# Kernel tuning notes

Measured on AMD Instinct MI355X. Metric: run time of the kernel, lower is better.

## Reference

```python
import jax, jax.numpy as jnp
import numpy as np

N = 100000   # nodes
E = 640000   # edges
D = 128      # in_channels
C = 40       # out_channels (classes)


def setup_inputs() -> dict:
    key = jax.random.key(0)
    ks = jax.random.split(key, 6)
    x = jax.random.normal(ks[0], (N, D), jnp.float32)
    edge_index = jax.random.randint(ks[1], (2, E), 0, N)
    edge_weight = jax.random.uniform(ks[2], (E,), jnp.float32)
    # 8 block convs (4 blocks x 2) stacked, + final conv
    Wb = jax.random.normal(ks[3], (8, D, D), jnp.float32) / np.sqrt(D)
    bb = jnp.zeros((8, D), jnp.float32)
    Wf = jax.random.normal(ks[4], (D, C), jnp.float32) / np.sqrt(D)
    bf = jnp.zeros((C,), jnp.float32)
    return dict(x=x, edge_index=edge_index, edge_weight=edge_weight,
                Wb=Wb, bb=bb, Wf=Wf, bf=bf)


def _gcn(x, W, b, src, dst, w):
    """PyG GCNConv (normalize=True) with self-loops already appended to src/dst/w."""
    n = x.shape[0]
    h = x @ W                                   # [N, out]
    deg = jax.ops.segment_sum(w, dst, num_segments=n)
    dinv = jnp.where(deg > 0, jax.lax.rsqrt(deg), 0.0)
    norm = dinv[src] * w * dinv[dst]            # [E+N]
    out = jax.ops.segment_sum(h[src] * norm[:, None], dst, num_segments=n)
    return out + b


def reference(x, edge_index, edge_weight, Wb, bb, Wf, bf):
    n = x.shape[0]
    loop = jnp.arange(n)
    src = jnp.concatenate([edge_index[0], loop])
    dst = jnp.concatenate([edge_index[1], loop])
    w = jnp.concatenate([edge_weight, jnp.ones((n,), x.dtype)])
    # forward only runs blocks 1-4 (blocks 5-7 unused in the original forward)
    for i in range(4):
        identity = x
        x = jax.nn.relu(_gcn(x, Wb[2 * i], bb[2 * i], src, dst, w))
        # dropout: identity in eval mode
        x = jax.nn.relu(_gcn(x, Wb[2 * i + 1], bb[2 * i + 1], src, dst, w))
        # F.normalize: row-wise L2 with eps=1e-12
        x = x / jnp.maximum(jnp.linalg.norm(x, axis=1, keepdims=True), 1e-12)
        x = (x + identity) / 2
    x = _gcn(x, Wf, bf, src, dst, w)
    return jax.nn.log_softmax(x, axis=1)
```

## Files before the change

kernel.cpp:

```cpp
#include <hip/hip_runtime.h>
#include <math.h>

#define NN 100000
#define EE 640000
#define DD 128
#define CC 40
#define FIXS 4194304.0f

typedef __bf16 bf16x8 __attribute__((ext_vector_type(8)));
typedef float f32x4 __attribute__((ext_vector_type(4)));
typedef unsigned short us8 __attribute__((ext_vector_type(8)));

__device__ inline unsigned short f2b(float f) {
    union { float f; unsigned u; } v; v.f = f;
    unsigned u = v.u;
    return (unsigned short)((u + 0x7FFFu + ((u >> 16) & 1u)) >> 16);
}
__device__ inline float b2f(unsigned short b) {
    union { unsigned u; float f; } v; v.u = ((unsigned)b) << 16;
    return v.f;
}


__global__ __launch_bounds__(256) void k_edge1(const int* __restrict__ dst,
                                               const float* __restrict__ w,
                                               unsigned long long* __restrict__ degcnt,
                                               int* __restrict__ pos) {
    int e = blockIdx.x * 256 + threadIdx.x;
    if (e < EE) {
        int d = dst[e];
        unsigned long long pk =
            ((unsigned long long)(unsigned)(w[e] * FIXS) << 32) | 1ull;
        unsigned long long old = atomicAdd(&degcnt[d], pk);
        pos[e] = (int)(old & 0xffffffffull);
    }
}

__global__ __launch_bounds__(256) void k_scan1(const unsigned long long* __restrict__ degcnt,
                                               float* __restrict__ dinv,
                                               int* __restrict__ out,
                                               int* __restrict__ partial) {
    __shared__ int lds[256];
    int t = threadIdx.x;
    int base = blockIdx.x * 1024 + t * 4;
    int v[4]; int s = 0;
    #pragma unroll
    for (int j = 0; j < 4; ++j) {
        int idx = base + j;
        unsigned long long dc = (idx < NN) ? degcnt[idx] : 0ull;
        v[j] = (int)(dc & 0xffffffffull);
        s += v[j];
        if (idx < NN)
            dinv[idx] = rsqrtf((float)(unsigned)(dc >> 32) * (1.0f / FIXS) + 1.0f);
    }
    lds[t] = s;
    __syncthreads();
    for (int off = 1; off < 256; off <<= 1) {
        int x = lds[t];
        int y = (t >= off) ? lds[t - off] : 0;
        __syncthreads();
        lds[t] = x + y;
        __syncthreads();
    }
    int excl = lds[t] - s;
    if (t == 255) partial[blockIdx.x] = lds[255];
    int run = excl;
    #pragma unroll
    for (int j = 0; j < 4; ++j) {
        int idx = base + j;
        if (idx < NN) out[idx] = run;
        run += v[j];
    }
}

__global__ __launch_bounds__(128) void k_scan2(int* __restrict__ partial) {
    __shared__ int lds[128];
    int t = threadIdx.x;
    int v = (t < 98) ? partial[t] : 0;
    lds[t] = v;
    __syncthreads();
    for (int off = 1; off < 128; off <<= 1) {
        int x = lds[t];
        int y = (t >= off) ? lds[t - off] : 0;
        __syncthreads();
        lds[t] = x + y;
        __syncthreads();
    }
    if (t < 98) partial[t] = lds[t] - v;
}

__global__ __launch_bounds__(256) void k_scan3(int* __restrict__ rp,
                                               const int* __restrict__ partial) {
    int i = blockIdx.x * 256 + threadIdx.x;
    if (i < NN) rp[i] += partial[i >> 10];
    if (i == 0) rp[NN] = EE;
}

__global__ __launch_bounds__(256) void k_scatter(const int* __restrict__ src,
                                                 const int* __restrict__ dst,
                                                 const float* __restrict__ w,
                                                 const float* __restrict__ dinv,
                                                 const int* __restrict__ rp,
                                                 const int* __restrict__ pos,
                                                 int* __restrict__ col,
                                                 float* __restrict__ val) {
    int e = blockIdx.x * 256 + threadIdx.x;
    if (e < EE) {
        int s = src[e], d = dst[e];
        int p = rp[d] + pos[e];
        col[p] = s;
        val[p] = dinv[s] * w[e] * dinv[d];
    }
}


__global__ __launch_bounds__(256) void k_prep_w(const float* __restrict__ Wb,
                                                unsigned short* __restrict__ WT) {
    int idx = blockIdx.x * 256 + threadIdx.x;
    if (idx >= 8 * DD * DD) return;
    int m = idx >> 14;
    int n = (idx >> 7) & 127;
    int k = idx & 127;
    WT[idx] = f2b(Wb[(size_t)m * DD * DD + (size_t)k * DD + n]);
}

__global__ __launch_bounds__(256) void k_prep_wf(const float* __restrict__ Wf,
                                                 unsigned short* __restrict__ WfT) {
    int idx = blockIdx.x * 256 + threadIdx.x;
    if (idx >= 64 * DD) return;
    int n = idx >> 7;
    int k = idx & 127;
    WfT[idx] = (n < CC) ? f2b(Wf[(size_t)k * CC + n]) : 0;
}

__global__ __launch_bounds__(256) void k_x2bf(const float* __restrict__ x,
                                              unsigned short* __restrict__ Abf) {
    int idx = blockIdx.x * 256 + threadIdx.x;
    if (idx >= NN * DD / 4) return;
    float4 v = ((const float4*)x)[idx];
    ushort4 r;
    r.x = f2b(v.x); r.y = f2b(v.y); r.z = f2b(v.z); r.w = f2b(v.w);
    ((ushort4*)Abf)[idx] = r;
}

__global__ __launch_bounds__(256) void k_mm_mfma(const unsigned short* __restrict__ X,
                                                 const unsigned short* __restrict__ WT,
                                                 unsigned short* __restrict__ H) {
    int wid = threadIdx.x >> 6;
    int lane = threadIdx.x & 63;
    int r0 = blockIdx.x * 64 + wid * 16;
    int sl = lane & 15, g = lane >> 4;
    int arow = r0 + sl;
    if (arow >= NN) arow = NN - 1;

    f32x4 acc[8];
    #pragma unroll
    for (int n = 0; n < 8; ++n) acc[n] = (f32x4){0.f, 0.f, 0.f, 0.f};

    const bf16x8* xrow = (const bf16x8*)(X + (size_t)arow * DD);
    #pragma unroll
    for (int kc = 0; kc < 4; ++kc) {
        bf16x8 a = xrow[kc * 4 + g];
        #pragma unroll
        for (int n = 0; n < 8; ++n) {
            const bf16x8* wrow = (const bf16x8*)(WT + (size_t)(n * 16 + sl) * DD);
            bf16x8 b = wrow[kc * 4 + g];
            acc[n] = __builtin_amdgcn_mfma_f32_16x16x32_bf16(a, b, acc[n], 0, 0, 0);
        }
    }
    #pragma unroll
    for (int n = 0; n < 8; ++n) {
        #pragma unroll
        for (int v = 0; v < 4; ++v) {
            int row = r0 + g * 4 + v;
            if (row < NN) H[(size_t)row * DD + n * 16 + sl] = f2b(acc[n][v]);
        }
    }
}

__global__ __launch_bounds__(256) void k_mm40b(const unsigned short* __restrict__ X,
                                               const unsigned short* __restrict__ WfT,
                                               unsigned short* __restrict__ H) {
    int wid = threadIdx.x >> 6;
    int lane = threadIdx.x & 63;
    int r0 = blockIdx.x * 64 + wid * 16;
    int sl = lane & 15, g = lane >> 4;
    int arow = r0 + sl;
    if (arow >= NN) arow = NN - 1;

    f32x4 acc[4];
    #pragma unroll
    for (int n = 0; n < 4; ++n) acc[n] = (f32x4){0.f, 0.f, 0.f, 0.f};

    const bf16x8* xrow = (const bf16x8*)(X + (size_t)arow * DD);
    #pragma unroll
    for (int kc = 0; kc < 4; ++kc) {
        bf16x8 a = xrow[kc * 4 + g];
        #pragma unroll
        for (int n = 0; n < 4; ++n) {
            const bf16x8* wrow = (const bf16x8*)(WfT + (size_t)(n * 16 + sl) * DD);
            bf16x8 b = wrow[kc * 4 + g];
            acc[n] = __builtin_amdgcn_mfma_f32_16x16x32_bf16(a, b, acc[n], 0, 0, 0);
        }
    }
    #pragma unroll
    for (int n = 0; n < 4; ++n) {
        #pragma unroll
        for (int v = 0; v < 4; ++v) {
            int row = r0 + g * 4 + v;
            if (row < NN) H[(size_t)row * 64 + n * 16 + sl] = f2b(acc[n][v]);
        }
    }
}


#define AGG_CORE(h_, node_, sl_, a_, STRIDE_)                               \
    {                                                                       \
        float dv = dinv[node_];                                             \
        float dv2 = dv * dv;                                                \
        us8 m_ = ((const us8*)(h_ + (size_t)node_ * STRIDE_))[sl_];         \
        _Pragma("unroll")                                                   \
        for (int j = 0; j < 8; ++j) a_[j] = dv2 * b2f(m_[j]);               \
        int e = rp[node_], end = rp[node_ + 1];                             \
        for (; e + 4 <= end; e += 4) {                                      \
            int s0 = col[e], s1 = col[e + 1], s2 = col[e + 2], s3 = col[e + 3]; \
            float v0 = val[e], v1 = val[e + 1], v2 = val[e + 2], v3 = val[e + 3]; \
            us8 q0 = ((const us8*)(h_ + (size_t)s0 * STRIDE_))[sl_];        \
            us8 q1 = ((const us8*)(h_ + (size_t)s1 * STRIDE_))[sl_];        \
            us8 q2 = ((const us8*)(h_ + (size_t)s2 * STRIDE_))[sl_];        \
            us8 q3 = ((const us8*)(h_ + (size_t)s3 * STRIDE_))[sl_];        \
            _Pragma("unroll")                                               \
            for (int j = 0; j < 8; ++j)                                     \
                a_[j] += (v0 * b2f(q0[j]) + v1 * b2f(q1[j]))                \
                       + (v2 * b2f(q2[j]) + v3 * b2f(q3[j]));               \
        }                                                                   \
        for (; e < end; ++e) {                                              \
            int s0 = col[e];                                                \
            float v0 = val[e];                                              \
            us8 q0 = ((const us8*)(h_ + (size_t)s0 * STRIDE_))[sl_];        \
            _Pragma("unroll")                                               \
            for (int j = 0; j < 8; ++j) a_[j] += v0 * b2f(q0[j]);           \
        }                                                                   \
    }

__global__ __launch_bounds__(256) void k_agg128(const unsigned short* __restrict__ h,
                                                const float* __restrict__ dinv,
                                                const int* __restrict__ rp,
                                                const int* __restrict__ col,
                                                const float* __restrict__ val,
                                                const float* __restrict__ bias,
                                                unsigned short* __restrict__ outb) {
    int node = blockIdx.x * 16 + (threadIdx.x >> 4);
    int sl = threadIdx.x & 15;
    if (node >= NN) return;
    float a[8];
    AGG_CORE(h, node, sl, a, DD);
    float4 bz0 = ((const float4*)bias)[sl * 2];
    float4 bz1 = ((const float4*)bias)[sl * 2 + 1];
    float bb[8] = {bz0.x, bz0.y, bz0.z, bz0.w, bz1.x, bz1.y, bz1.z, bz1.w};
    us8 r;
    #pragma unroll
    for (int j = 0; j < 8; ++j) r[j] = f2b(fmaxf(a[j] + bb[j], 0.f));
    ((us8*)(outb + (size_t)node * DD))[sl] = r;
}

__global__ __launch_bounds__(256) void k_agg128_nr(const unsigned short* __restrict__ h,
                                                   const float* __restrict__ dinv,
                                                   const int* __restrict__ rp,
                                                   const int* __restrict__ col,
                                                   const float* __restrict__ val,
                                                   const float* __restrict__ bias,
                                                   unsigned short* __restrict__ Abf) {
    int node = blockIdx.x * 16 + (threadIdx.x >> 4);
    int sl = threadIdx.x & 15;
    if (node >= NN) return;
    float a[8];
    AGG_CORE(h, node, sl, a, DD);
    float4 bz0 = ((const float4*)bias)[sl * 2];
    float4 bz1 = ((const float4*)bias)[sl * 2 + 1];
    float bb[8] = {bz0.x, bz0.y, bz0.z, bz0.w, bz1.x, bz1.y, bz1.z, bz1.w};
    float ss = 0.f;
    #pragma unroll
    for (int j = 0; j < 8; ++j) {
        a[j] = fmaxf(a[j] + bb[j], 0.f);
        ss += a[j] * a[j];
    }
    ss += __shfl_xor(ss, 1);
    ss += __shfl_xor(ss, 2);
    ss += __shfl_xor(ss, 4);
    ss += __shfl_xor(ss, 8);
    float sc = 1.0f / fmaxf(sqrtf(ss), 1e-12f);
    us8 oldb = ((const us8*)(Abf + (size_t)node * DD))[sl];
    us8 rb;
    #pragma unroll
    for (int j = 0; j < 8; ++j)
        rb[j] = f2b((a[j] * sc + b2f(oldb[j])) * 0.5f);
    ((us8*)(Abf + (size_t)node * DD))[sl] = rb;
}

__global__ __launch_bounds__(256) void k_agg_final(const unsigned short* __restrict__ h,
                                                   const float* __restrict__ dinv,
                                                   const int* __restrict__ rp,
                                                   const int* __restrict__ col,
                                                   const float* __restrict__ val,
                                                   const float* __restrict__ bias,
                                                   float* __restrict__ out) {
    int node = blockIdx.x * 32 + (threadIdx.x >> 3);
    int sl = threadIdx.x & 7;
    if (node >= NN) return;
    float a[8];
    AGG_CORE(h, node, sl, a, 64);
    bool real = sl < 5;
    float vv[8];
    if (real) {
        float4 bz0 = ((const float4*)bias)[sl * 2];
        float4 bz1 = ((const float4*)bias)[sl * 2 + 1];
        float bb[8] = {bz0.x, bz0.y, bz0.z, bz0.w, bz1.x, bz1.y, bz1.z, bz1.w};
        #pragma unroll
        for (int j = 0; j < 8; ++j) vv[j] = a[j] + bb[j];
    } else {
        #pragma unroll
        for (int j = 0; j < 8; ++j) vv[j] = -3.0e38f;
    }
    float m = vv[0];
    #pragma unroll
    for (int j = 1; j < 8; ++j) m = fmaxf(m, vv[j]);
    m = fmaxf(m, __shfl_xor(m, 1));
    m = fmaxf(m, __shfl_xor(m, 2));
    m = fmaxf(m, __shfl_xor(m, 4));
    float s = 0.f;
    if (real) {
        #pragma unroll
        for (int j = 0; j < 8; ++j) s += expf(vv[j] - m);
    }
    s += __shfl_xor(s, 1);
    s += __shfl_xor(s, 2);
    s += __shfl_xor(s, 4);
    float ls = m + logf(s);
    if (real) {
        float4 o0 = {vv[0] - ls, vv[1] - ls, vv[2] - ls, vv[3] - ls};
        float4 o1 = {vv[4] - ls, vv[5] - ls, vv[6] - ls, vv[7] - ls};
        float* orow = out + (size_t)node * CC + sl * 8;
        *(float4*)(orow) = o0;
        *(float4*)(orow + 4) = o1;
    }
}


extern "C" void kernel_launch(void* const* d_in, const int* in_sizes, int n_in,
                              void* d_out, int out_size, void* d_ws, size_t ws_size,
                              hipStream_t stream) {
    const float* x  = (const float*)d_in[0];
    const int*   ei = (const int*)d_in[1];
    const float* ew = (const float*)d_in[2];
    const float* Wb = (const float*)d_in[3];
    const float* bb = (const float*)d_in[4];
    const float* Wf = (const float*)d_in[5];
    const float* bf_ = (const float*)d_in[6];
    const int* src = ei;
    const int* dst = ei + EE;
    float* out = (float*)d_out;

    char* p = (char*)d_ws;
    unsigned short*     Abf    = (unsigned short*)p;     p += (size_t)NN * DD * 2;
    unsigned short*     Bbf    = (unsigned short*)p;     p += (size_t)NN * DD * 2;
    unsigned short*     Cbf    = (unsigned short*)p;     p += (size_t)NN * DD * 2;
    unsigned short*     H48    = (unsigned short*)p;     p += (size_t)NN * 64 * 2;
    unsigned short*     WT     = (unsigned short*)p;     p += (size_t)8 * DD * DD * 2;
    unsigned short*     WfT    = (unsigned short*)p;     p += (size_t)64 * DD * 2;
    unsigned long long* degcnt = (unsigned long long*)p; p += (size_t)NN * 8;
    float* dinv = (float*)p; p += (size_t)NN * 4;
    int*   rp   = (int*)p;   p += (size_t)(NN + 1) * 4;
    int*   pos  = (int*)p;   p += (size_t)EE * 4;
    int*   col  = (int*)p;   p += (size_t)EE * 4;
    float* val  = (float*)p; p += (size_t)EE * 4;
    int*   partial = (int*)p; p += 128 * 4;

    hipMemsetAsync(degcnt, 0, (size_t)NN * 8, stream);

    k_edge1<<<(EE + 255) / 256, 256, 0, stream>>>(dst, ew, degcnt, pos);
    k_scan1<<<98, 256, 0, stream>>>(degcnt, dinv, rp, partial);
    k_scan2<<<1, 128, 0, stream>>>(partial);
    k_scan3<<<(NN + 255) / 256, 256, 0, stream>>>(rp, partial);
    k_scatter<<<(EE + 255) / 256, 256, 0, stream>>>(src, dst, ew, dinv, rp, pos, col, val);

    k_prep_w<<<(8 * DD * DD + 255) / 256, 256, 0, stream>>>(Wb, WT);
    k_prep_wf<<<(64 * DD + 255) / 256, 256, 0, stream>>>(Wf, WfT);
    k_x2bf<<<(NN * DD / 4 + 255) / 256, 256, 0, stream>>>(x, Abf);

    for (int blk = 0; blk < 4; ++blk) {
        k_mm_mfma<<<(NN + 63) / 64, 256, 0, stream>>>(Abf, WT + (size_t)(2 * blk) * DD * DD, Bbf);
        k_agg128<<<(NN + 15) / 16, 256, 0, stream>>>(Bbf, dinv, rp, col, val, bb + (size_t)(2 * blk) * DD, Cbf);
        k_mm_mfma<<<(NN + 63) / 64, 256, 0, stream>>>(Cbf, WT + (size_t)(2 * blk + 1) * DD * DD, Bbf);
        k_agg128_nr<<<(NN + 15) / 16, 256, 0, stream>>>(Bbf, dinv, rp, col, val, bb + (size_t)(2 * blk + 1) * DD, Abf);
    }
    k_mm40b<<<(NN + 63) / 64, 256, 0, stream>>>(Abf, WfT, H48);
    k_agg_final<<<(NN + 31) / 32, 256, 0, stream>>>(H48, dinv, rp, col, val, bf_, out);
}
```

Before: 666.0 us.

## Fuse aggregation with the next layer's MFMA matmul through shared memory

Each aggregation kernel now writes its 64-node output tile into LDS and immediately multiplies it by the next layer's weight with MFMA. This removes the separate matmul kernels and the round trip of the intermediate activation through global memory. The input conversion is fused with the first matmul, and the two weight-prep kernels are merged into one. Aggregation blocks now cover 64 nodes in four serial rounds instead of 16 nodes, which lowers parallelism per block and may lengthen the tail caused by uneven node degrees.

```diff
diff --git a/kernel.cpp b/kernel.cpp
--- a/kernel.cpp
+++ b/kernel.cpp
@@ -113,105 +113,55 @@
     }
 }
 
-
-__global__ __launch_bounds__(256) void k_prep_w(const float* __restrict__ Wb,
-                                                unsigned short* __restrict__ WT) {
+__global__ __launch_bounds__(256) void k_prep(const float* __restrict__ Wb,
+                                              const float* __restrict__ Wf,
+                                              unsigned short* __restrict__ WT,
+                                              unsigned short* __restrict__ WfT) {
     int idx = blockIdx.x * 256 + threadIdx.x;
-    if (idx >= 8 * DD * DD) return;
-    int m = idx >> 14;
-    int n = (idx >> 7) & 127;
-    int k = idx & 127;
-    WT[idx] = f2b(Wb[(size_t)m * DD * DD + (size_t)k * DD + n]);
-}
-
-__global__ __launch_bounds__(256) void k_prep_wf(const float* __restrict__ Wf,
-                                                 unsigned short* __restrict__ WfT) {
-    int idx = blockIdx.x * 256 + threadIdx.x;
-    if (idx >= 64 * DD) return;
-    int n = idx >> 7;
-    int k = idx & 127;
-    WfT[idx] = (n < CC) ? f2b(Wf[(size_t)k * CC + n]) : 0;
-}
-
-__global__ __launch_bounds__(256) void k_x2bf(const float* __restrict__ x,
-                                              unsigned short* __restrict__ Abf) {
-    int idx = blockIdx.x * 256 + threadIdx.x;
-    if (idx >= NN * DD / 4) return;
-    float4 v = ((const float4*)x)[idx];
-    ushort4 r;
-    r.x = f2b(v.x); r.y = f2b(v.y); r.z = f2b(v.z); r.w = f2b(v.w);
-    ((ushort4*)Abf)[idx] = r;
-}
-
-__global__ __launch_bounds__(256) void k_mm_mfma(const unsigned short* __restrict__ X,
-                                                 const unsigned short* __restrict__ WT,
-                                                 unsigned short* __restrict__ H) {
-    int wid = threadIdx.x >> 6;
-    int lane = threadIdx.x & 63;
-    int r0 = blockIdx.x * 64 + wid * 16;
-    int sl = lane & 15, g = lane >> 4;
-    int arow = r0 + sl;
-    if (arow >= NN) arow = NN - 1;
-
-    f32x4 acc[8];
-    #pragma unroll
-    for (int n = 0; n < 8; ++n) acc[n] = (f32x4){0.f, 0.f, 0.f, 0.f};
-
-    const bf16x8* xrow = (const bf16x8*)(X + (size_t)arow * DD);
-    #pragma unroll
-    for (int kc = 0; kc < 4; ++kc) {
-        bf16x8 a = xrow[kc * 4 + g];
-        #pragma unroll
-        for (int n = 0; n < 8; ++n) {
-            const bf16x8* wrow = (const bf16x8*)(WT + (size_t)(n * 16 + sl) * DD);
-            bf16x8 b = wrow[kc * 4 + g];
-            acc[n] = __builtin_amdgcn_mfma_f32_16x16x32_bf16(a, b, acc[n], 0, 0, 0);
-        }
-    }
-    #pragma unroll
-    for (int n = 0; n < 8; ++n) {
-        #pragma unroll
-        for (int v = 0; v < 4; ++v) {
-            int row = r0 + g * 4 + v;
-            if (row < NN) H[(size_t)row * DD + n * 16 + sl] = f2b(acc[n][v]);
-        }
-    }
-}
-
-__global__ __launch_bounds__(256) void k_mm40b(const unsigned short* __restrict__ X,
-                                               const unsigned short* __restrict__ WfT,
-                                               unsigned short* __restrict__ H) {
-    int wid = threadIdx.x >> 6;
-    int lane = threadIdx.x & 63;
-    int r0 = blockIdx.x * 64 + wid * 16;
-    int sl = lane & 15, g = lane >> 4;
-    int arow = r0 + sl;
-    if (arow >= NN) arow = NN - 1;
-
-    f32x4 acc[4];
-    #pragma unroll
-    for (int n = 0; n < 4; ++n) acc[n] = (f32x4){0.f, 0.f, 0.f, 0.f};
-
-    const bf16x8* xrow = (const bf16x8*)(X + (size_t)arow * DD);
-    #pragma unroll
-    for (int kc = 0; kc < 4; ++kc) {
-        bf16x8 a = xrow[kc * 4 + g];
-        #pragma unroll
-        for (int n = 0; n < 4; ++n) {
-            const bf16x8* wrow = (const bf16x8*)(WfT + (size_t)(n * 16 + sl) * DD);
-            bf16x8 b = wrow[kc * 4 + g];
-            acc[n] = __builtin_amdgcn_mfma_f32_16x16x32_bf16(a, b, acc[n], 0, 0, 0);
-        }
-    }
-    #pragma unroll
-    for (int n = 0; n < 4; ++n) {
-        #pragma unroll
-        for (int v = 0; v < 4; ++v) {
-            int row = r0 + g * 4 + v;
-            if (row < NN) H[(size_t)row * 64 + n * 16 + sl] = f2b(acc[n][v]);
-        }
-    }
-}
+    if (idx < 8 * DD * DD) {
+        int m = idx >> 14;
+        int n = (idx >> 7) & 127;
+        int k = idx & 127;
+        WT[idx] = f2b(Wb[(size_t)m * DD * DD + (size_t)k * DD + n]);
+    } else {
+        int j = idx - 8 * DD * DD;
+        if (j < 64 * DD) {
+            int n = j >> 7;
+            int k = j & 127;
+            WfT[j] = (n < CC) ? f2b(Wf[(size_t)k * CC + n]) : 0;
+        }
+    }
+}
+
+
+#define MFMA_PHASE(WT_, H_)                                                  \
+    {                                                                        \
+        int wid = threadIdx.x >> 6;                                          \
+        int lane = threadIdx.x & 63;                                         \
+        int msl = lane & 15, g = lane >> 4;                                  \
+        int r0 = node0 + wid * 16;                                           \
+        f32x4 acc[8];                                                        \
+        _Pragma("unroll")                                                    \
+        for (int n = 0; n < 8; ++n) acc[n] = (f32x4){0.f, 0.f, 0.f, 0.f};    \
+        _Pragma("unroll")                                                    \
+        for (int kc = 0; kc < 4; ++kc) {                                     \
+            bf16x8 a = *(const bf16x8*)(&xs[wid * 16 + msl][kc * 32 + g * 8]); \
+            _Pragma("unroll")                                                \
+            for (int n = 0; n < 8; ++n) {                                    \
+                const bf16x8* wrow = (const bf16x8*)(WT_ + (size_t)(n * 16 + msl) * DD); \
+                bf16x8 b = wrow[kc * 4 + g];                                 \
+                acc[n] = __builtin_amdgcn_mfma_f32_16x16x32_bf16(a, b, acc[n], 0, 0, 0); \
+            }                                                                \
+        }                                                                    \
+        _Pragma("unroll")                                                    \
+        for (int n = 0; n < 8; ++n) {                                        \
+            _Pragma("unroll")                                                \
+            for (int v = 0; v < 4; ++v) {                                    \
+                int row = r0 + g * 4 + v;                                    \
+                if (row < NN) H_[(size_t)row * DD + n * 16 + msl] = f2b(acc[n][v]); \
+            }                                                                \
+        }                                                                    \
+    }
 
 
 #define AGG_CORE(h_, node_, sl_, a_, STRIDE_)                               \
@@ -243,25 +193,113 @@
         }                                                                   \
     }
 
-__global__ __launch_bounds__(256) void k_agg128(const unsigned short* __restrict__ h,
-                                                const float* __restrict__ dinv,
-                                                const int* __restrict__ rp,
-                                                const int* __restrict__ col,
-                                                const float* __restrict__ val,
-                                                const float* __restrict__ bias,
-                                                unsigned short* __restrict__ outb) {
-    int node = blockIdx.x * 16 + (threadIdx.x >> 4);
+
+__global__ __launch_bounds__(256) void k_xmm(const float* __restrict__ x,
+                                             const unsigned short* __restrict__ WT,
+                                             unsigned short* __restrict__ Abf,
+                                             unsigned short* __restrict__ H) {
+    __shared__ unsigned short xs[64][136];
+    int node0 = blockIdx.x * 64;
     int sl = threadIdx.x & 15;
-    if (node >= NN) return;
-    float a[8];
-    AGG_CORE(h, node, sl, a, DD);
-    float4 bz0 = ((const float4*)bias)[sl * 2];
-    float4 bz1 = ((const float4*)bias)[sl * 2 + 1];
-    float bb[8] = {bz0.x, bz0.y, bz0.z, bz0.w, bz1.x, bz1.y, bz1.z, bz1.w};
-    us8 r;
-    #pragma unroll
-    for (int j = 0; j < 8; ++j) r[j] = f2b(fmaxf(a[j] + bb[j], 0.f));
-    ((us8*)(outb + (size_t)node * DD))[sl] = r;
+    int grp = threadIdx.x >> 4;
+    for (int rnd = 0; rnd < 4; ++rnd) {
+        int node = node0 + rnd * 16 + grp;
+        us8 r;
+        if (node < NN) {
+            float4 v0 = *(const float4*)(x + (size_t)node * DD + sl * 8);
+            float4 v1 = *(const float4*)(x + (size_t)node * DD + sl * 8 + 4);
+            r[0] = f2b(v0.x); r[1] = f2b(v0.y); r[2] = f2b(v0.z); r[3] = f2b(v0.w);
+            r[4] = f2b(v1.x); r[5] = f2b(v1.y); r[6] = f2b(v1.z); r[7] = f2b(v1.w);
+            ((us8*)(Abf + (size_t)node * DD))[sl] = r;
+        } else {
+            #pragma unroll
+            for (int j = 0; j < 8; ++j) r[j] = 0;
+        }
+        *(us8*)(&xs[rnd * 16 + grp][sl * 8]) = r;
+    }
+    __syncthreads();
+    MFMA_PHASE(WT, H);
+}
+
+__global__ __launch_bounds__(256) void k_aggmm(const unsigned short* __restrict__ h,
+                                               const float* __restrict__ dinv,
+                                               const int* __restrict__ rp,
+                                               const int* __restrict__ col,
+                                               const float* __restrict__ val,
+                                               const float* __restrict__ bias,
+                                               const unsigned short* __restrict__ WTn,
+                                               unsigned short* __restrict__ H) {
+    __shared__ unsigned short xs[64][136];
+    int node0 = blockIdx.x * 64;
+    int sl = threadIdx.x & 15;
+    int grp = threadIdx.x >> 4;
+    for (int rnd = 0; rnd < 4; ++rnd) {
+        int node = node0 + rnd * 16 + grp;
+        us8 r;
+        if (node < NN) {
+            float a[8];
+            AGG_CORE(h, node, sl, a, DD);
+            float4 bz0 = ((const float4*)bias)[sl * 2];
+            float4 bz1 = ((const float4*)bias)[sl * 2 + 1];
+            float bb[8] = {bz0.x, bz0.y, bz0.z, bz0.w, bz1.x, bz1.y, bz1.z, bz1.w};
+            #pragma unroll
+            for (int j = 0; j < 8; ++j) r[j] = f2b(fmaxf(a[j] + bb[j], 0.f));
+        } else {
+            #pragma unroll
+            for (int j = 0; j < 8; ++j) r[j] = 0;
+        }
+        *(us8*)(&xs[rnd * 16 + grp][sl * 8]) = r;
+    }
+    __syncthreads();
+    MFMA_PHASE(WTn, H);
+}
+
+__global__ __launch_bounds__(256) void k_aggnr_mm(const unsigned short* __restrict__ h,
+                                                  const float* __restrict__ dinv,
+                                                  const int* __restrict__ rp,
+                                                  const int* __restrict__ col,
+                                                  const float* __restrict__ val,
+                                                  const float* __restrict__ bias,
+                                                  unsigned short* __restrict__ Abf,
+                                                  const unsigned short* __restrict__ WTn,
+                                                  unsigned short* __restrict__ H) {
+    __shared__ unsigned short xs[64][136];
+    int node0 = blockIdx.x * 64;
+    int sl = threadIdx.x & 15;
+    int grp = threadIdx.x >> 4;
+    for (int rnd = 0; rnd < 4; ++rnd) {
+        int node = node0 + rnd * 16 + grp;
+        us8 rb;
+        if (node < NN) {
+            float a[8];
+            AGG_CORE(h, node, sl, a, DD);
+            float4 bz0 = ((const float4*)bias)[sl * 2];
+            float4 bz1 = ((const float4*)bias)[sl * 2 + 1];
+            float bb[8] = {bz0.x, bz0.y, bz0.z, bz0.w, bz1.x, bz1.y, bz1.z, bz1.w};
+            float ss = 0.f;
+            #pragma unroll
+            for (int j = 0; j < 8; ++j) {
+                a[j] = fmaxf(a[j] + bb[j], 0.f);
+                ss += a[j] * a[j];
+            }
+            ss += __shfl_xor(ss, 1);
+            ss += __shfl_xor(ss, 2);
+            ss += __shfl_xor(ss, 4);
+            ss += __shfl_xor(ss, 8);
+            float sc = 1.0f / fmaxf(sqrtf(ss), 1e-12f);
+            us8 oldb = ((const us8*)(Abf + (size_t)node * DD))[sl];
+            #pragma unroll
+            for (int j = 0; j < 8; ++j)
+                rb[j] = f2b((a[j] * sc + b2f(oldb[j])) * 0.5f);
+            ((us8*)(Abf + (size_t)node * DD))[sl] = rb;
+        } else {
+            #pragma unroll
+            for (int j = 0; j < 8; ++j) rb[j] = 0;
+        }
+        *(us8*)(&xs[rnd * 16 + grp][sl * 8]) = rb;
+    }
+    __syncthreads();
+    MFMA_PHASE(WTn, H);
 }
 
 __global__ __launch_bounds__(256) void k_agg128_nr(const unsigned short* __restrict__ h,
@@ -296,6 +334,41 @@
     for (int j = 0; j < 8; ++j)
         rb[j] = f2b((a[j] * sc + b2f(oldb[j])) * 0.5f);
     ((us8*)(Abf + (size_t)node * DD))[sl] = rb;
+}
+
+__global__ __launch_bounds__(256) void k_mm40b(const unsigned short* __restrict__ X,
+                                               const unsigned short* __restrict__ WfT,
+                                               unsigned short* __restrict__ H) {
+    int wid = threadIdx.x >> 6;
+    int lane = threadIdx.x & 63;
+    int r0 = blockIdx.x * 64 + wid * 16;
+    int sl = lane & 15, g = lane >> 4;
+    int arow = r0 + sl;
+    if (arow >= NN) arow = NN - 1;
+
+    f32x4 acc[4];
+    #pragma unroll
+    for (int n = 0; n < 4; ++n) acc[n] = (f32x4){0.f, 0.f, 0.f, 0.f};
+
+    const bf16x8* xrow = (const bf16x8*)(X + (size_t)arow * DD);
+    #pragma unroll
+    for (int kc = 0; kc < 4; ++kc) {
+        bf16x8 a = xrow[kc * 4 + g];
+        #pragma unroll
+        for (int n = 0; n < 4; ++n) {
+            const bf16x8* wrow = (const bf16x8*)(WfT + (size_t)(n * 16 + sl) * DD);
+            bf16x8 b = wrow[kc * 4 + g];
+            acc[n] = __builtin_amdgcn_mfma_f32_16x16x32_bf16(a, b, acc[n], 0, 0, 0);
+        }
+    }
+    #pragma unroll
+    for (int n = 0; n < 4; ++n) {
+        #pragma unroll
+        for (int v = 0; v < 4; ++v) {
+            int row = r0 + g * 4 + v;
+            if (row < NN) H[(size_t)row * 64 + n * 16 + sl] = f2b(acc[n][v]);
+        }
+    }
 }
 
 __global__ __launch_bounds__(256) void k_agg_final(const unsigned short* __restrict__ h,
@@ -364,7 +437,7 @@
     char* p = (char*)d_ws;
     unsigned short*     Abf    = (unsigned short*)p;     p += (size_t)NN * DD * 2;
     unsigned short*     Bbf    = (unsigned short*)p;     p += (size_t)NN * DD * 2;
-    unsigned short*     Cbf    = (unsigned short*)p;     p += (size_t)NN * DD * 2;
+    unsigned short*     B2     = (unsigned short*)p;     p += (size_t)NN * DD * 2;
     unsigned short*     H48    = (unsigned short*)p;     p += (size_t)NN * 64 * 2;
     unsigned short*     WT     = (unsigned short*)p;     p += (size_t)8 * DD * DD * 2;
     unsigned short*     WfT    = (unsigned short*)p;     p += (size_t)64 * DD * 2;
@@ -383,17 +456,23 @@
     k_scan2<<<1, 128, 0, stream>>>(partial);
     k_scan3<<<(NN + 255) / 256, 256, 0, stream>>>(rp, partial);
     k_scatter<<<(EE + 255) / 256, 256, 0, stream>>>(src, dst, ew, dinv, rp, pos, col, val);
-
-    k_prep_w<<<(8 * DD * DD + 255) / 256, 256, 0, stream>>>(Wb, WT);
-    k_prep_wf<<<(64 * DD + 255) / 256, 256, 0, stream>>>(Wf, WfT);
-    k_x2bf<<<(NN * DD / 4 + 255) / 256, 256, 0, stream>>>(x, Abf);
-
+    k_prep<<<(8 * DD * DD + 64 * DD + 255) / 256, 256, 0, stream>>>(Wb, Wf, WT, WfT);
+
+    int gb = (NN + 63) / 64;
+    k_xmm<<<gb, 256, 0, stream>>>(x, WT, Abf, Bbf);
     for (int blk = 0; blk < 4; ++blk) {
-        k_mm_mfma<<<(NN + 63) / 64, 256, 0, stream>>>(Abf, WT + (size_t)(2 * blk) * DD * DD, Bbf);
-        k_agg128<<<(NN + 15) / 16, 256, 0, stream>>>(Bbf, dinv, rp, col, val, bb + (size_t)(2 * blk) * DD, Cbf);
-        k_mm_mfma<<<(NN + 63) / 64, 256, 0, stream>>>(Cbf, WT + (size_t)(2 * blk + 1) * DD * DD, Bbf);
-        k_agg128_nr<<<(NN + 15) / 16, 256, 0, stream>>>(Bbf, dinv, rp, col, val, bb + (size_t)(2 * blk + 1) * DD, Abf);
-    }
-    k_mm40b<<<(NN + 63) / 64, 256, 0, stream>>>(Abf, WfT, H48);
+        k_aggmm<<<gb, 256, 0, stream>>>(Bbf, dinv, rp, col, val,
+                                        bb + (size_t)(2 * blk) * DD,
+                                        WT + (size_t)(2 * blk + 1) * DD * DD, B2);
+        if (blk < 3) {
+            k_aggnr_mm<<<gb, 256, 0, stream>>>(B2, dinv, rp, col, val,
+                                               bb + (size_t)(2 * blk + 1) * DD, Abf,
+                                               WT + (size_t)(2 * blk + 2) * DD * DD, Bbf);
+        } else {
+            k_agg128_nr<<<(NN + 15) / 16, 256, 0, stream>>>(B2, dinv, rp, col, val,
+                                                            bb + (size_t)(2 * blk + 1) * DD, Abf);
+        }
+    }
+    k_mm40b<<<gb, 256, 0, stream>>>(Abf, WfT, H48);
     k_agg_final<<<(NN + 31) / 32, 256, 0, stream>>>(H48, dinv, rp, col, val, bf_, out);
 }
```

Measured after the change: 672.5 us. No clear change (+1.0%).

## Fuse x-to-bf16 conversion into first matmul, merge weight prep, widen gather batch

Applied to the files above, without the earlier changes.

Merges the two weight-transpose kernels into one launch. Fuses the fp32-to-bf16 conversion of x with the first block's MFMA matmul through shared memory, so x is not re-read from bf16 global memory. Rewrites the aggregation core to gather 8 neighbours per iteration with masked, clamped indices and no scalar tail loop. This adds memory-level parallelism but wastes some loads and FMAs on low-degree nodes.

```diff
diff --git a/kernel.cpp b/kernel.cpp
--- a/kernel.cpp
+++ b/kernel.cpp
@@ -113,35 +113,110 @@
     }
 }
 
-
-__global__ __launch_bounds__(256) void k_prep_w(const float* __restrict__ Wb,
-                                                unsigned short* __restrict__ WT) {
+__global__ __launch_bounds__(256) void k_prep(const float* __restrict__ Wb,
+                                              const float* __restrict__ Wf,
+                                              unsigned short* __restrict__ WT,
+                                              unsigned short* __restrict__ WfT) {
     int idx = blockIdx.x * 256 + threadIdx.x;
-    if (idx >= 8 * DD * DD) return;
-    int m = idx >> 14;
-    int n = (idx >> 7) & 127;
-    int k = idx & 127;
-    WT[idx] = f2b(Wb[(size_t)m * DD * DD + (size_t)k * DD + n]);
-}
-
-__global__ __launch_bounds__(256) void k_prep_wf(const float* __restrict__ Wf,
-                                                 unsigned short* __restrict__ WfT) {
-    int idx = blockIdx.x * 256 + threadIdx.x;
-    if (idx >= 64 * DD) return;
-    int n = idx >> 7;
-    int k = idx & 127;
-    WfT[idx] = (n < CC) ? f2b(Wf[(size_t)k * CC + n]) : 0;
-}
-
-__global__ __launch_bounds__(256) void k_x2bf(const float* __restrict__ x,
-                                              unsigned short* __restrict__ Abf) {
-    int idx = blockIdx.x * 256 + threadIdx.x;
-    if (idx >= NN * DD / 4) return;
-    float4 v = ((const float4*)x)[idx];
-    ushort4 r;
-    r.x = f2b(v.x); r.y = f2b(v.y); r.z = f2b(v.z); r.w = f2b(v.w);
-    ((ushort4*)Abf)[idx] = r;
-}
+    if (idx < 8 * DD * DD) {
+        int m = idx >> 14;
+        int n = (idx >> 7) & 127;
+        int k = idx & 127;
+        WT[idx] = f2b(Wb[(size_t)m * DD * DD + (size_t)k * DD + n]);
+    } else {
+        int j = idx - 8 * DD * DD;
+        if (j < 64 * DD) {
+            int n = j >> 7;
+            int k = j & 127;
+            WfT[j] = (n < CC) ? f2b(Wf[(size_t)k * CC + n]) : 0;
+        }
+    }
+}
+
+
+#define AGG_CORE(h_, node_, sl_, a_, STRIDE_)                               \
+    {                                                                       \
+        float dv = dinv[node_];                                             \
+        float dv2 = dv * dv;                                                \
+        us8 m_ = ((const us8*)(h_ + (size_t)node_ * STRIDE_))[sl_];         \
+        _Pragma("unroll")                                                   \
+        for (int j = 0; j < 8; ++j) a_[j] = dv2 * b2f(m_[j]);               \
+        int e0 = rp[node_], e1 = rp[node_ + 1];                             \
+        for (int base = e0; base < e1; base += 8) {                         \
+            us8 q_[8]; float w_[8];                                         \
+            _Pragma("unroll")                                               \
+            for (int j = 0; j < 8; ++j) {                                   \
+                int idx = base + j;                                         \
+                bool ok = idx < e1;                                         \
+                int cidx = ok ? idx : e0;                                   \
+                w_[j] = ok ? val[cidx] : 0.f;                               \
+                q_[j] = ((const us8*)(h_ + (size_t)col[cidx] * STRIDE_))[sl_]; \
+            }                                                               \
+            _Pragma("unroll")                                               \
+            for (int j = 0; j < 8; ++j) {                                   \
+                _Pragma("unroll")                                           \
+                for (int k2 = 0; k2 < 8; ++k2)                              \
+                    a_[k2] += w_[j] * b2f(q_[j][k2]);                       \
+            }                                                               \
+        }                                                                   \
+    }
+
+
+typedef f32x4 f32x4_t;
+
+__global__ __launch_bounds__(256) void k_xmm(const float* __restrict__ x,
+                                             const unsigned short* __restrict__ WT,
+                                             unsigned short* __restrict__ Abf,
+                                             unsigned short* __restrict__ H) {
+    __shared__ unsigned short xs[64][136];
+    int node0 = blockIdx.x * 64;
+    int sl = threadIdx.x & 15;
+    int grp = threadIdx.x >> 4;
+    for (int rnd = 0; rnd < 4; ++rnd) {
+        int node = node0 + rnd * 16 + grp;
+        us8 r;
+        if (node < NN) {
+            float4 v0 = *(const float4*)(x + (size_t)node * DD + sl * 8);
+            float4 v1 = *(const float4*)(x + (size_t)node * DD + sl * 8 + 4);
+            r[0] = f2b(v0.x); r[1] = f2b(v0.y); r[2] = f2b(v0.z); r[3] = f2b(v0.w);
+            r[4] = f2b(v1.x); r[5] = f2b(v1.y); r[6] = f2b(v1.z); r[7] = f2b(v1.w);
+            ((us8*)(Abf + (size_t)node * DD))[sl] = r;
+        } else {
+            #pragma unroll
+            for (int j = 0; j < 8; ++j) r[j] = 0;
+        }
+        *(us8*)(&xs[rnd * 16 + grp][sl * 8]) = r;
+    }
+    __syncthreads();
+    {
+        int wid = threadIdx.x >> 6;
+        int lane = threadIdx.x & 63;
+        int msl = lane & 15, g = lane >> 4;
+        int r0 = node0 + wid * 16;
+        f32x4 acc[8];
+        #pragma unroll
+        for (int n = 0; n < 8; ++n) acc[n] = (f32x4){0.f, 0.f, 0.f, 0.f};
+        #pragma unroll
+        for (int kc = 0; kc < 4; ++kc) {
+            bf16x8 a = *(const bf16x8*)(&xs[wid * 16 + msl][kc * 32 + g * 8]);
+            #pragma unroll
+            for (int n = 0; n < 8; ++n) {
+                const bf16x8* wrow = (const bf16x8*)(WT + (size_t)(n * 16 + msl) * DD);
+                bf16x8 b = wrow[kc * 4 + g];
+                acc[n] = __builtin_amdgcn_mfma_f32_16x16x32_bf16(a, b, acc[n], 0, 0, 0);
+            }
+        }
+        #pragma unroll
+        for (int n = 0; n < 8; ++n) {
+            #pragma unroll
+            for (int v = 0; v < 4; ++v) {
+                int row = r0 + g * 4 + v;
+                if (row < NN) H[(size_t)row * DD + n * 16 + msl] = f2b(acc[n][v]);
+            }
+        }
+    }
+}
+
 
 __global__ __launch_bounds__(256) void k_mm_mfma(const unsigned short* __restrict__ X,
                                                  const unsigned short* __restrict__ WT,
@@ -213,35 +288,6 @@
     }
 }
 
-
-#define AGG_CORE(h_, node_, sl_, a_, STRIDE_)                               \
-    {                                                                       \
-        float dv = dinv[node_];                                             \
-        float dv2 = dv * dv;                                                \
-        us8 m_ = ((const us8*)(h_ + (size_t)node_ * STRIDE_))[sl_];         \
-        _Pragma("unroll")                                                   \
-        for (int j = 0; j < 8; ++j) a_[j] = dv2 * b2f(m_[j]);               \
-        int e = rp[node_], end = rp[node_ + 1];                             \
-        for (; e + 4 <= end; e += 4) {                                      \
-            int s0 = col[e], s1 = col[e + 1], s2 = col[e + 2], s3 = col[e + 3]; \
-            float v0 = val[e], v1 = val[e + 1], v2 = val[e + 2], v3 = val[e + 3]; \
-            us8 q0 = ((const us8*)(h_ + (size_t)s0 * STRIDE_))[sl_];        \
-            us8 q1 = ((const us8*)(h_ + (size_t)s1 * STRIDE_))[sl_];        \
-            us8 q2 = ((const us8*)(h_ + (size_t)s2 * STRIDE_))[sl_];        \
-            us8 q3 = ((const us8*)(h_ + (size_t)s3 * STRIDE_))[sl_];        \
-            _Pragma("unroll")                                               \
-            for (int j = 0; j < 8; ++j)                                     \
-                a_[j] += (v0 * b2f(q0[j]) + v1 * b2f(q1[j]))                \
-                       + (v2 * b2f(q2[j]) + v3 * b2f(q3[j]));               \
-        }                                                                   \
-        for (; e < end; ++e) {                                              \
-            int s0 = col[e];                                                \
-            float v0 = val[e];                                              \
-            us8 q0 = ((const us8*)(h_ + (size_t)s0 * STRIDE_))[sl_];        \
-            _Pragma("unroll")                                               \
-            for (int j = 0; j < 8; ++j) a_[j] += v0 * b2f(q0[j]);           \
-        }                                                                   \
-    }
 
 __global__ __launch_bounds__(256) void k_agg128(const unsigned short* __restrict__ h,
                                                 const float* __restrict__ dinv,
@@ -383,17 +429,19 @@
     k_scan2<<<1, 128, 0, stream>>>(partial);
     k_scan3<<<(NN + 255) / 256, 256, 0, stream>>>(rp, partial);
     k_scatter<<<(EE + 255) / 256, 256, 0, stream>>>(src, dst, ew, dinv, rp, pos, col, val);
-
-    k_prep_w<<<(8 * DD * DD + 255) / 256, 256, 0, stream>>>(Wb, WT);
-    k_prep_wf<<<(64 * DD + 255) / 256, 256, 0, stream>>>(Wf, WfT);
-    k_x2bf<<<(NN * DD / 4 + 255) / 256, 256, 0, stream>>>(x, Abf);
-
+    k_prep<<<(8 * DD * DD + 64 * DD + 255) / 256, 256, 0, stream>>>(Wb, Wf, WT, WfT);
+
+    int gb = (NN + 63) / 64;
+    k_xmm<<<gb, 256, 0, stream>>>(x, WT, Abf, Bbf);
     for (int blk = 0; blk < 4; ++blk) {
-        k_mm_mfma<<<(NN + 63) / 64, 256, 0, stream>>>(Abf, WT + (size_t)(2 * blk) * DD * DD, Bbf);
-        k_agg128<<<(NN + 15) / 16, 256, 0, stream>>>(Bbf, dinv, rp, col, val, bb + (size_t)(2 * blk) * DD, Cbf);
-        k_mm_mfma<<<(NN + 63) / 64, 256, 0, stream>>>(Cbf, WT + (size_t)(2 * blk + 1) * DD * DD, Bbf);
-        k_agg128_nr<<<(NN + 15) / 16, 256, 0, stream>>>(Bbf, dinv, rp, col, val, bb + (size_t)(2 * blk + 1) * DD, Abf);
-    }
-    k_mm40b<<<(NN + 63) / 64, 256, 0, stream>>>(Abf, WfT, H48);
+        k_agg128<<<(NN + 15) / 16, 256, 0, stream>>>(Bbf, dinv, rp, col, val,
+                                                     bb + (size_t)(2 * blk) * DD, Cbf);
+        k_mm_mfma<<<gb, 256, 0, stream>>>(Cbf, WT + (size_t)(2 * blk + 1) * DD * DD, Bbf);
+        k_agg128_nr<<<(NN + 15) / 16, 256, 0, stream>>>(Bbf, dinv, rp, col, val,
+                                                        bb + (size_t)(2 * blk + 1) * DD, Abf);
+        if (blk < 3)
+            k_mm_mfma<<<gb, 256, 0, stream>>>(Abf, WT + (size_t)(2 * blk + 2) * DD * DD, Bbf);
+    }
+    k_mm40b<<<gb, 256, 0, stream>>>(Abf, WfT, H48);
     k_agg_final<<<(NN + 31) / 32, 256, 0, stream>>>(H48, dinv, rp, col, val, bf_, out);
 }
```

New measurement: 751.9 us. 1.13x slower.
